# Kernel optimization log

Hardware: AMD Instinct MI355X
Metric: run time of the kernel (lower is better)

The kernel has to match this reference:

```python
import jax, jax.numpy as jnp
import numpy as np

B, T, C, H = 2, 2048, 1024, 16
D = C // H  # head_dim = 64


def setup_inputs() -> dict:
    key = jax.random.key(0)
    ks = jax.random.split(key, 5)
    x = jax.random.normal(ks[0], (B, T, C), dtype=jnp.float32)
    # fused QKV projection: Linear(C, 3C)
    W_qkv = jax.random.normal(ks[1], (C, 3 * C), dtype=jnp.float32) / np.sqrt(C)
    b_qkv = jax.random.normal(ks[2], (3 * C,), dtype=jnp.float32) * 0.02
    # output projection: Linear(C, C)
    W_proj = jax.random.normal(ks[3], (C, C), dtype=jnp.float32) / np.sqrt(C)
    b_proj = jax.random.normal(ks[4], (C,), dtype=jnp.float32) * 0.02
    return {"x": x, "W_qkv": W_qkv, "b_qkv": b_qkv, "W_proj": W_proj, "b_proj": b_proj}


def reference(x, W_qkv, b_qkv, W_proj, b_proj):
    # fused QKV projection
    qkv = jnp.einsum("btc,cd->btd", x, W_qkv) + b_qkv  # [B,T,3C]
    q, k, v = jnp.split(qkv, 3, axis=-1)
    # [B,T,C] -> [B,H,T,D]
    def to_heads(t):
        return t.reshape(B, T, H, D).transpose(0, 2, 1, 3)
    q, k, v = to_heads(q), to_heads(k), to_heads(v)
    # causal scaled dot-product attention (SDPA default scale = 1/sqrt(head_dim))
    scale = 1.0 / np.sqrt(D).astype(np.float32)
    scores = jnp.einsum("bhqd,bhkd->bhqk", q, k) * scale  # [B,H,T,T]
    causal = jnp.tril(jnp.ones((T, T), dtype=bool))
    scores = jnp.where(causal, scores, jnp.finfo(scores.dtype).min)
    attn = jax.nn.softmax(scores, axis=-1)
    out = jnp.einsum("bhqk,bhkd->bhqd", attn, v)  # [B,H,T,D]
    out = out.transpose(0, 2, 1, 3).reshape(B, T, C)
    # output projection
    return jnp.einsum("btc,cd->btd", out, W_proj) + b_proj
```

## Files before the change

kernel.cpp:

```cpp
#include <hip/hip_runtime.h>
#include <hip/hip_bf16.h>

typedef __attribute__((ext_vector_type(8))) __bf16 bf16x8;
typedef __attribute__((ext_vector_type(8))) short short8;
typedef __attribute__((ext_vector_type(4))) float f32x4;
typedef __attribute__((ext_vector_type(16))) float f32x16;
typedef __attribute__((ext_vector_type(4))) short sh4;

typedef __attribute__((address_space(1))) void GVoid;
typedef __attribute__((address_space(3))) void LVoid;

#define NEGBIG (-1e30f)
#define SCL 0.18033688011112042f

constexpr int TT = 2048, CC = 1024, HH = 16, DD = 64, C3 = 3072;

__device__ __forceinline__ unsigned short f2bf(float f) {
  unsigned int i = __float_as_uint(f);
  return (unsigned short)((i + 0x7FFFu + ((i >> 16) & 1u)) >> 16);
}
__device__ __forceinline__ void async16(const void* g, void* l) {
  __builtin_amdgcn_global_load_lds((GVoid*)g, (LVoid*)l, 16, 0, 0);
}

__global__ __launch_bounds__(256) void cvt_bf16(
    const float* __restrict__ in, unsigned short* __restrict__ out, int n8)
{
  const int i = blockIdx.x * 256 + threadIdx.x;
  if (i >= n8) return;
  const float* p = in + (size_t)i * 8;
  f32x4 a = *(const f32x4*)p, b = *(const f32x4*)(p + 4);
  sh4 r0, r1;
  ((unsigned short*)&r0)[0] = f2bf(a[0]); ((unsigned short*)&r0)[1] = f2bf(a[1]);
  ((unsigned short*)&r0)[2] = f2bf(a[2]); ((unsigned short*)&r0)[3] = f2bf(a[3]);
  ((unsigned short*)&r1)[0] = f2bf(b[0]); ((unsigned short*)&r1)[1] = f2bf(b[1]);
  ((unsigned short*)&r1)[2] = f2bf(b[2]); ((unsigned short*)&r1)[3] = f2bf(b[3]);
  *(sh4*)(out + (size_t)i * 8) = r0;
  *(sh4*)(out + (size_t)i * 8 + 4) = r1;
}

__global__ __launch_bounds__(256) void transpose_cvt(
    const float* __restrict__ in, unsigned short* __restrict__ out, int R, int Cd)
{
  __shared__ __align__(16) unsigned short tile[64 * 72];
  const int r0 = blockIdx.y * 64, c0 = blockIdx.x * 64;
  const int tid = threadIdx.x;
#pragma unroll
  for (int r = 0; r < 2; ++r) {
    const int elem = r * 2048 + tid * 8;
    const int ii = elem >> 6, jj = elem & 63;
    const float* p = in + (size_t)(r0 + ii) * Cd + c0 + jj;
    f32x4 a = *(const f32x4*)p, b = *(const f32x4*)(p + 4);
    short8 v;
    ((unsigned short*)&v)[0] = f2bf(a[0]); ((unsigned short*)&v)[1] = f2bf(a[1]);
    ((unsigned short*)&v)[2] = f2bf(a[2]); ((unsigned short*)&v)[3] = f2bf(a[3]);
    ((unsigned short*)&v)[4] = f2bf(b[0]); ((unsigned short*)&v)[5] = f2bf(b[1]);
    ((unsigned short*)&v)[6] = f2bf(b[2]); ((unsigned short*)&v)[7] = f2bf(b[3]);
    *(short8*)&tile[ii * 72 + jj] = v;
  }
  __syncthreads();
#pragma unroll
  for (int r = 0; r < 2; ++r) {
    const int elem = r * 2048 + tid * 8;
    const int jj = elem >> 6, ii0 = elem & 63;
    short8 v;
#pragma unroll
    for (int e = 0; e < 8; ++e) ((unsigned short*)&v)[e] = tile[(ii0 + e) * 72 + jj];
    *(short8*)&out[(size_t)(c0 + jj) * R + r0 + ii0] = v;
  }
}

template <int MODE>
__global__ __launch_bounds__(256) void gemm_bt(
    const unsigned short* __restrict__ A,
    const unsigned short* __restrict__ Bt,
    const float* __restrict__ bias,
    void* __restrict__ Cp, unsigned short* __restrict__ Vt,
    int M, int N, int K, int lda)
{
  __shared__ __align__(16) unsigned short sA[128 * 32];
  __shared__ __align__(16) unsigned short sB[128 * 32];
  const int tid = threadIdx.x;
  const int w = tid >> 6, l = tid & 63, ln = l & 15, quad = l >> 4;
  const int wm = w >> 1, wn = w & 1;
  const int m0 = blockIdx.y * 128, n0 = blockIdx.x * 128;
  f32x4 acc[4][4] = {};

  for (int k0 = 0; k0 < K; k0 += 32) {
    __syncthreads();
#pragma unroll
    for (int r = 0; r < 2; ++r) {
      const int elem = r * 2048 + tid * 8;
      const int ar = elem >> 5, ac = elem & 31;
      async16(A  + (size_t)(m0 + ar) * lda + k0 + ac, sA + r * 2048 + w * 512);
      async16(Bt + (size_t)(n0 + ar) * K   + k0 + ac, sB + r * 2048 + w * 512);
    }
    __syncthreads();

    bf16x8 af[4], bfr[4];
#pragma unroll
    for (int i = 0; i < 4; i++)
      af[i] = *(const bf16x8*)&sA[(wm * 64 + i * 16 + ln) * 32 + quad * 8];
#pragma unroll
    for (int j = 0; j < 4; j++)
      bfr[j] = *(const bf16x8*)&sB[(wn * 64 + j * 16 + ln) * 32 + quad * 8];
#pragma unroll
    for (int i = 0; i < 4; i++)
#pragma unroll
      for (int j = 0; j < 4; j++)
        acc[i][j] = __builtin_amdgcn_mfma_f32_16x16x32_bf16(af[i], bfr[j], acc[i][j], 0, 0, 0);
  }

  float bj[4];
#pragma unroll
  for (int j = 0; j < 4; j++) bj[j] = bias[n0 + wn * 64 + j * 16 + ln];

#pragma unroll
  for (int i = 0; i < 4; i++) {
#pragma unroll
    for (int j = 0; j < 4; j++) {
      const int gn = n0 + wn * 64 + j * 16 + ln;
      if (MODE == 0 && gn >= 2048) {
        const int hh = (gn >> 6) & 15, dd = gn & 63;
        const int gm0 = m0 + wm * 64 + i * 16 + quad * 4;
        const int bb = gm0 >> 11, t0 = gm0 & 2047;
        sh4 rv;
#pragma unroll
        for (int g = 0; g < 4; ++g)
          ((unsigned short*)&rv)[g] = f2bf(acc[i][j][g] + bj[j]);
        *(sh4*)&Vt[((size_t)((bb * HH + hh) * DD + dd)) * TT + t0] = rv;
      } else {
#pragma unroll
        for (int g = 0; g < 4; ++g) {
          const int gm = m0 + wm * 64 + i * 16 + quad * 4 + g;
          float v = acc[i][j][g] + bj[j];
          if (MODE == 0) {
            if (gn < 1024) v *= SCL;
            ((unsigned short*)Cp)[(size_t)gm * 2048 + gn] = f2bf(v);
          } else {
            ((float*)Cp)[(size_t)gm * N + gn] = v;
          }
        }
      }
    }
  }
}

__global__ __launch_bounds__(256) void gemm_n64(
    const unsigned short* __restrict__ A,
    const unsigned short* __restrict__ Bt,
    const float* __restrict__ bias,
    float* __restrict__ Cp, int M, int N, int K, int lda)
{
  __shared__ __align__(16) unsigned short sA[128 * 32];
  __shared__ __align__(16) unsigned short sB[64 * 32];
  const int tid = threadIdx.x;
  const int w = tid >> 6, l = tid & 63, ln = l & 15, quad = l >> 4;
  const int wm = w >> 1, wn = w & 1;
  const int m0 = blockIdx.y * 128, n0 = blockIdx.x * 64;
  f32x4 acc[4][2] = {};

  for (int k0 = 0; k0 < K; k0 += 32) {
    __syncthreads();
#pragma unroll
    for (int r = 0; r < 2; ++r) {
      const int elem = r * 2048 + tid * 8;
      const int ar = elem >> 5, ac = elem & 31;
      async16(A + (size_t)(m0 + ar) * lda + k0 + ac, sA + r * 2048 + w * 512);
    }
    {
      const int elem = tid * 8;
      const int ar = elem >> 5, ac = elem & 31;
      async16(Bt + (size_t)(n0 + ar) * K + k0 + ac, sB + w * 512);
    }
    __syncthreads();

    bf16x8 af[4], bfr[2];
#pragma unroll
    for (int i = 0; i < 4; i++)
      af[i] = *(const bf16x8*)&sA[(wm * 64 + i * 16 + ln) * 32 + quad * 8];
#pragma unroll
    for (int j = 0; j < 2; j++)
      bfr[j] = *(const bf16x8*)&sB[(wn * 32 + j * 16 + ln) * 32 + quad * 8];
#pragma unroll
    for (int i = 0; i < 4; i++)
#pragma unroll
      for (int j = 0; j < 2; j++)
        acc[i][j] = __builtin_amdgcn_mfma_f32_16x16x32_bf16(af[i], bfr[j], acc[i][j], 0, 0, 0);
  }

  float bj[2];
#pragma unroll
  for (int j = 0; j < 2; j++) bj[j] = bias[n0 + wn * 32 + j * 16 + ln];

#pragma unroll
  for (int i = 0; i < 4; i++)
#pragma unroll
    for (int g = 0; g < 4; ++g) {
      const int gm = m0 + wm * 64 + i * 16 + quad * 4 + g;
#pragma unroll
      for (int j = 0; j < 2; j++) {
        const int gn = n0 + wn * 32 + j * 16 + ln;
        Cp[(size_t)gm * N + gn] = acc[i][j][g] + bj[j];
      }
    }
}

__global__ __launch_bounds__(512) void attn2g(
    unsigned short* __restrict__ QK, const unsigned short* __restrict__ Vt)
{
  __shared__ __align__(16) unsigned short kt[2][2][64 * 72];
  __shared__ __align__(16) unsigned short vt[2][3][64 * 72];
  __shared__ float Ox[4][2][16][64];
  __shared__ float Lx[4][64];
  const int pair = blockIdx.x, bh = blockIdx.y;
  const int b = bh >> 4, h = bh & 15;
  const int tid = threadIdx.x;
  const int grp = tid >> 8, gtid = tid & 255;
  const int wg = (tid >> 6) & 3, l = tid & 63;
  const int c = l & 31, h2 = l >> 5;
  unsigned short*       Qp = QK + (size_t)b * TT * 2048 + h * DD;
  const unsigned short* Kp = QK + (size_t)b * TT * 2048 + CC + h * DD;
  const unsigned short* Vh = Vt + (size_t)bh * DD * TT;
  const int si0 = gtid >> 3, so = (gtid & 7) * 8;

  for (int ph = 0; ph < 2; ++ph) {
    const int qt = ph ? 15 - pair : pair;
    const int qbase = qt * 128 + wg * 32;
    const int qm = qbase + c - 4 * h2;
    bf16x8 qv[4];
#pragma unroll
    for (int ds = 0; ds < 4; ++ds)
      qv[ds] = *(const bf16x8*)&Qp[(size_t)(qbase + c) * 2048 + ds * 16 + h2 * 8];

    f32x16 oacc[2] = {};
    bf16x8 pA[4] = {};
    float lsum = 0.0f;
    const int nslot = qt + 1;
    int vm1 = 2, v0 = 0, vp1 = 1;

    __syncthreads();
#pragma unroll
    for (int r = 0; r < 2; ++r) {
      const int si = si0 + 32 * r;
      *(short8*)&kt[grp][0][si * 72 + so] =
          *(const short8*)&Kp[(size_t)(grp * 64 + si) * 2048 + so];
      *(short8*)&vt[grp][0][si * 72 + so] =
          *(const short8*)&Vh[(size_t)si * TT + grp * 64 + so];
    }
    __syncthreads();

    for (int slot = 0; slot < nslot; ++slot) {
      const int kb = 2 * slot + grp;
      const int ck = slot & 1;
      short8 pk[2], pv[2];
      if (slot + 1 < nslot) {
        const int kbn = kb + 2;
#pragma unroll
        for (int r = 0; r < 2; ++r) {
          const int si = si0 + 32 * r;
          pk[r] = *(const short8*)&Kp[(size_t)(kbn * 64 + si) * 2048 + so];
          pv[r] = *(const short8*)&Vh[(size_t)si * TT + kbn * 64 + so];
        }
      }
      const bool qk_act = (kb * 64 <= qbase + 31);
      f32x16 sacc[2];
      if (qk_act) {
#pragma unroll
        for (int kg = 0; kg < 2; ++kg) {
          f32x16 sa = {};
#pragma unroll
          for (int ds = 0; ds < 4; ++ds) {
            bf16x8 kf = *(const bf16x8*)&kt[grp][ck][(kg * 32 + c) * 72 + ds * 16 + h2 * 8];
            sa = __builtin_amdgcn_mfma_f32_32x32x16_bf16(kf, qv[ds], sa, 0, 0, 0);
          }
          sacc[kg] = sa;
        }
      }
      if (slot > 0 && (kb - 2) * 64 <= qbase + 31) {
        const unsigned short* vp = vt[grp][vm1];
#pragma unroll
        for (int dg = 0; dg < 2; ++dg)
#pragma unroll
          for (int ks = 0; ks < 4; ++ks) {
            bf16x8 vf = *(const bf16x8*)&vp[(dg * 32 + c) * 72 + ks * 16 + h2 * 8];
            oacc[dg] = __builtin_amdgcn_mfma_f32_32x32x16_bf16(pA[ks], vf, oacc[dg], 0, 0, 0);
          }
      }
      if (qk_act) {
        const bool need_mask = (kb * 64 + 63 > qbase);
        float pe[2][16];
#pragma unroll
        for (int kg = 0; kg < 2; ++kg)
#pragma unroll
          for (int rr = 0; rr < 16; ++rr) {
            float sv = sacc[kg][rr];
            if (need_mask) {
              const int krel = kb * 64 + kg * 32 + (rr & 3) + 8 * (rr >> 2);
              if (krel > qm) sv = NEGBIG;
            }
            float e;
            asm("v_exp_f32 %0, %1" : "=v"(e) : "v"(sv));
            pe[kg][rr] = e;
            lsum += e;
          }
        unsigned W0[2][4], W1[2][4];
#pragma unroll
        for (int kg = 0; kg < 2; ++kg)
#pragma unroll
          for (int r4 = 0; r4 < 4; ++r4) {
            asm("v_cvt_pk_bf16_f32 %0, %1, %2"
                : "=v"(W0[kg][r4]) : "v"(pe[kg][4 * r4 + 0]), "v"(pe[kg][4 * r4 + 1]));
            asm("v_cvt_pk_bf16_f32 %0, %1, %2"
                : "=v"(W1[kg][r4]) : "v"(pe[kg][4 * r4 + 2]), "v"(pe[kg][4 * r4 + 3]));
          }
#pragma unroll
        for (int ks = 0; ks < 4; ++ks) {
          const int kg = ks >> 1, sel = ks & 1;
          unsigned a0 = W0[kg][2 * sel], b0 = W0[kg][2 * sel + 1];
          unsigned a1 = W1[kg][2 * sel], b1 = W1[kg][2 * sel + 1];
          asm("v_permlane32_swap_b32 %0, %1" : "+v"(a0), "+v"(b0));
          asm("v_permlane32_swap_b32 %0, %1" : "+v"(a1), "+v"(b1));
          unsigned wds[4] = {a0, a1, b0, b1};
          pA[ks] = *(const bf16x8*)wds;
        }
      }
      if (slot + 1 < nslot) {
#pragma unroll
        for (int r = 0; r < 2; ++r) {
          const int si = si0 + 32 * r;
          *(short8*)&kt[grp][1 - ck][si * 72 + so] = pk[r];
          *(short8*)&vt[grp][vp1][si * 72 + so] = pv[r];
        }
      }
      __syncthreads();
      const int t_ = vm1; vm1 = v0; v0 = vp1; vp1 = t_;
    }
    const int kb_last = 2 * qt + grp;
    if (kb_last * 64 <= qbase + 31) {
      const unsigned short* vp = vt[grp][vm1];
#pragma unroll
      for (int dg = 0; dg < 2; ++dg)
#pragma unroll
        for (int ks = 0; ks < 4; ++ks) {
          bf16x8 vf = *(const bf16x8*)&vp[(dg * 32 + c) * 72 + ks * 16 + h2 * 8];
          oacc[dg] = __builtin_amdgcn_mfma_f32_32x32x16_bf16(pA[ks], vf, oacc[dg], 0, 0, 0);
        }
    }
    lsum += __shfl_xor(lsum, 32);
    if (grp == 1) {
#pragma unroll
      for (int dg = 0; dg < 2; ++dg)
#pragma unroll
        for (int rr = 0; rr < 16; ++rr) Ox[wg][dg][rr][l] = oacc[dg][rr];
      Lx[wg][l] = lsum;
    }
    __syncthreads();
    if (grp == 0) {
      const float inv = 1.0f / (lsum + Lx[wg][l]);
#pragma unroll
      for (int dg = 0; dg < 2; ++dg)
#pragma unroll
        for (int rr = 0; rr < 16; ++rr) oacc[dg][rr] += Ox[wg][dg][rr][l];
#pragma unroll
      for (int rr = 0; rr < 16; ++rr) {
        const int q_rel = (rr & 3) + 8 * (rr >> 2) + 4 * h2;
        const float iq = __shfl(inv, q_rel);
        const size_t trow = qbase + q_rel;
#pragma unroll
        for (int dg = 0; dg < 2; ++dg)
          Qp[trow * 2048 + dg * 32 + c] = f2bf(oacc[dg][rr] * iq);
      }
    }
  }
}

extern "C" void kernel_launch(void* const* d_in, const int* in_sizes, int n_in,
                              void* d_out, int out_size, void* d_ws, size_t ws_size,
                              hipStream_t stream)
{
  (void)in_sizes; (void)n_in; (void)out_size; (void)ws_size;
  const float* x     = (const float*)d_in[0];
  const float* Wqkv  = (const float*)d_in[1];
  const float* bqkv  = (const float*)d_in[2];
  const float* Wproj = (const float*)d_in[3];
  const float* bproj = (const float*)d_in[4];

  unsigned short* QK     = (unsigned short*)d_ws;
  unsigned short* WqkvT  = QK + (size_t)4096 * 2048;
  unsigned short* WprojT = WqkvT;
  unsigned short* Vt = (unsigned short*)d_out;
  unsigned short* xb = Vt + (size_t)32 * 64 * 2048;

  cvt_bf16<<<dim3(4096 * 1024 / 8 / 256), 256, 0, stream>>>(x, xb, 4096 * 1024 / 8);
  transpose_cvt<<<dim3(C3 / 64, CC / 64), 256, 0, stream>>>(Wqkv, WqkvT, CC, C3);
  gemm_bt<0><<<dim3(C3 / 128, 4096 / 128), 256, 0, stream>>>(
      xb, WqkvT, bqkv, QK, Vt, 4096, C3, CC, CC);
  transpose_cvt<<<dim3(CC / 64, CC / 64), 256, 0, stream>>>(Wproj, WprojT, CC, CC);
  attn2g<<<dim3(8, 2 * HH), 512, 0, stream>>>(QK, Vt);
  gemm_n64<<<dim3(CC / 64, 4096 / 128), 256, 0, stream>>>(
      QK, WprojT, bproj, (float*)d_out, 4096, CC, CC, 2048);
}
```

Before: 185.7 us.

## Double-buffer LDS tiles in both projection GEMM kernels to prefetch next K-slice

Both GEMM kernels (the QKV projection and the narrow output projection) now keep two LDS buffers for their A and B tiles. The async global-to-LDS loads for the next K-slice are issued before the MFMA work on the current slice, and one barrier per iteration replaces the previous two. The goal is to hide global load latency behind the matrix math and cut barrier overhead. In exchange, LDS use per block doubles, which could reduce occupancy. The overlap is limited because the barrier likely waits for all outstanding loads before the next iteration starts.

```diff
diff --git a/kernel.cpp b/kernel.cpp
--- a/kernel.cpp
+++ b/kernel.cpp
@@ -78,37 +78,48 @@
     void* __restrict__ Cp, unsigned short* __restrict__ Vt,
     int M, int N, int K, int lda)
 {
-  __shared__ __align__(16) unsigned short sA[128 * 32];
-  __shared__ __align__(16) unsigned short sB[128 * 32];
+  __shared__ __align__(16) unsigned short sA[2][128 * 32];
+  __shared__ __align__(16) unsigned short sB[2][128 * 32];
   const int tid = threadIdx.x;
   const int w = tid >> 6, l = tid & 63, ln = l & 15, quad = l >> 4;
   const int wm = w >> 1, wn = w & 1;
   const int m0 = blockIdx.y * 128, n0 = blockIdx.x * 128;
   f32x4 acc[4][4] = {};
 
-  for (int k0 = 0; k0 < K; k0 += 32) {
-    __syncthreads();
-#pragma unroll
-    for (int r = 0; r < 2; ++r) {
-      const int elem = r * 2048 + tid * 8;
-      const int ar = elem >> 5, ac = elem & 31;
-      async16(A  + (size_t)(m0 + ar) * lda + k0 + ac, sA + r * 2048 + w * 512);
-      async16(Bt + (size_t)(n0 + ar) * K   + k0 + ac, sB + r * 2048 + w * 512);
-    }
-    __syncthreads();
+  const int elem0 = tid * 8;
+  const int ar0 = elem0 >> 5, ac0 = elem0 & 31;
+  const int ar1 = (2048 + elem0) >> 5, ac1 = ac0;
+
+  async16(A  + (size_t)(m0 + ar0) * lda + ac0, &sA[0][w * 512]);
+  async16(Bt + (size_t)(n0 + ar0) * K   + ac0, &sB[0][w * 512]);
+  async16(A  + (size_t)(m0 + ar1) * lda + ac1, &sA[0][2048 + w * 512]);
+  async16(Bt + (size_t)(n0 + ar1) * K   + ac1, &sB[0][2048 + w * 512]);
+  __syncthreads();
+
+  int buf = 0;
+  for (int k0 = 0; k0 < K; k0 += 32, buf ^= 1) {
+    if (k0 + 32 < K) {
+      const int nb = buf ^ 1, kn = k0 + 32;
+      async16(A  + (size_t)(m0 + ar0) * lda + kn + ac0, &sA[nb][w * 512]);
+      async16(Bt + (size_t)(n0 + ar0) * K   + kn + ac0, &sB[nb][w * 512]);
+      async16(A  + (size_t)(m0 + ar1) * lda + kn + ac1, &sA[nb][2048 + w * 512]);
+      async16(Bt + (size_t)(n0 + ar1) * K   + kn + ac1, &sB[nb][2048 + w * 512]);
+    }
 
     bf16x8 af[4], bfr[4];
 #pragma unroll
     for (int i = 0; i < 4; i++)
-      af[i] = *(const bf16x8*)&sA[(wm * 64 + i * 16 + ln) * 32 + quad * 8];
+      af[i] = *(const bf16x8*)&sA[buf][(wm * 64 + i * 16 + ln) * 32 + quad * 8];
 #pragma unroll
     for (int j = 0; j < 4; j++)
-      bfr[j] = *(const bf16x8*)&sB[(wn * 64 + j * 16 + ln) * 32 + quad * 8];
+      bfr[j] = *(const bf16x8*)&sB[buf][(wn * 64 + j * 16 + ln) * 32 + quad * 8];
 #pragma unroll
     for (int i = 0; i < 4; i++)
 #pragma unroll
       for (int j = 0; j < 4; j++)
         acc[i][j] = __builtin_amdgcn_mfma_f32_16x16x32_bf16(af[i], bfr[j], acc[i][j], 0, 0, 0);
+
+    __syncthreads();
   }
 
   float bj[4];
@@ -152,41 +163,46 @@
     const float* __restrict__ bias,
     float* __restrict__ Cp, int M, int N, int K, int lda)
 {
-  __shared__ __align__(16) unsigned short sA[128 * 32];
-  __shared__ __align__(16) unsigned short sB[64 * 32];
+  __shared__ __align__(16) unsigned short sA[2][128 * 32];
+  __shared__ __align__(16) unsigned short sB[2][64 * 32];
   const int tid = threadIdx.x;
   const int w = tid >> 6, l = tid & 63, ln = l & 15, quad = l >> 4;
   const int wm = w >> 1, wn = w & 1;
   const int m0 = blockIdx.y * 128, n0 = blockIdx.x * 64;
   f32x4 acc[4][2] = {};
 
-  for (int k0 = 0; k0 < K; k0 += 32) {
-    __syncthreads();
-#pragma unroll
-    for (int r = 0; r < 2; ++r) {
-      const int elem = r * 2048 + tid * 8;
-      const int ar = elem >> 5, ac = elem & 31;
-      async16(A + (size_t)(m0 + ar) * lda + k0 + ac, sA + r * 2048 + w * 512);
-    }
-    {
-      const int elem = tid * 8;
-      const int ar = elem >> 5, ac = elem & 31;
-      async16(Bt + (size_t)(n0 + ar) * K + k0 + ac, sB + w * 512);
-    }
-    __syncthreads();
+  const int elem0 = tid * 8;
+  const int ar0 = elem0 >> 5, ac0 = elem0 & 31;
+  const int ar1 = (2048 + elem0) >> 5, ac1 = ac0;
+
+  async16(A  + (size_t)(m0 + ar0) * lda + ac0, &sA[0][w * 512]);
+  async16(A  + (size_t)(m0 + ar1) * lda + ac1, &sA[0][2048 + w * 512]);
+  async16(Bt + (size_t)(n0 + ar0) * K   + ac0, &sB[0][w * 512]);
+  __syncthreads();
+
+  int buf = 0;
+  for (int k0 = 0; k0 < K; k0 += 32, buf ^= 1) {
+    if (k0 + 32 < K) {
+      const int nb = buf ^ 1, kn = k0 + 32;
+      async16(A  + (size_t)(m0 + ar0) * lda + kn + ac0, &sA[nb][w * 512]);
+      async16(A  + (size_t)(m0 + ar1) * lda + kn + ac1, &sA[nb][2048 + w * 512]);
+      async16(Bt + (size_t)(n0 + ar0) * K   + kn + ac0, &sB[nb][w * 512]);
+    }
 
     bf16x8 af[4], bfr[2];
 #pragma unroll
     for (int i = 0; i < 4; i++)
-      af[i] = *(const bf16x8*)&sA[(wm * 64 + i * 16 + ln) * 32 + quad * 8];
+      af[i] = *(const bf16x8*)&sA[buf][(wm * 64 + i * 16 + ln) * 32 + quad * 8];
 #pragma unroll
     for (int j = 0; j < 2; j++)
-      bfr[j] = *(const bf16x8*)&sB[(wn * 32 + j * 16 + ln) * 32 + quad * 8];
+      bfr[j] = *(const bf16x8*)&sB[buf][(wn * 32 + j * 16 + ln) * 32 + quad * 8];
 #pragma unroll
     for (int i = 0; i < 4; i++)
 #pragma unroll
       for (int j = 0; j < 2; j++)
         acc[i][j] = __builtin_amdgcn_mfma_f32_16x16x32_bf16(af[i], bfr[j], acc[i][j], 0, 0, 0);
+
+    __syncthreads();
   }
 
   float bj[2];
```

Result: faster. 180.4 us (-2.8%).
